# Kernel tuning notes

Measured on AMD Instinct MI355X. Metric: run time of the kernel, lower is better.

Reference implementation:

```python
import jax, jax.numpy as jnp
import numpy as np

B, T, D, H = 64, 1024, 512, 512

def setup_inputs() -> dict:
    key = jax.random.key(0)
    k1, k2, k3, k4 = jax.random.split(key, 4)
    x = jax.random.normal(k1, (B, T, D), dtype=jnp.float32)
    # Keras LSTM weights: kernel [D, 4H], recurrent_kernel [H, 4H], bias [4H]
    # gate order: i, f, c(g), o
    kernel = jax.random.normal(k2, (D, 4 * H), dtype=jnp.float32) * 0.05
    recurrent_kernel = jax.random.normal(k3, (H, 4 * H), dtype=jnp.float32) * 0.05
    bias = jax.random.normal(k4, (4 * H,), dtype=jnp.float32) * 0.05
    return {"x": x, "kernel": kernel, "recurrent_kernel": recurrent_kernel, "bias": bias}

def reference(x, kernel, recurrent_kernel, bias):
    # Precompute input projections for all timesteps: [B, T, 4H]
    xW = jnp.einsum('btd,dg->btg', x, kernel) + bias
    xW_t = jnp.transpose(xW, (1, 0, 2))  # [T, B, 4H] for scan over time
    h0 = jnp.zeros((x.shape[0], recurrent_kernel.shape[0]), dtype=x.dtype)
    c0 = jnp.zeros_like(h0)

    def step(carry, xw):
        h, c = carry
        z = xw + h @ recurrent_kernel  # [B, 4H]
        i, f, g, o = jnp.split(z, 4, axis=-1)
        i = jax.nn.sigmoid(i)
        f = jax.nn.sigmoid(f)
        g = jnp.tanh(g)
        o = jax.nn.sigmoid(o)
        c_new = f * c + i * g
        h_new = o * jnp.tanh(c_new)
        return (h_new, c_new), None

    (h_final, _), _ = jax.lax.scan(step, (h0, c0), xW_t)
    return h_final  # [B, H]
```

## Files before the change

### kernel.cpp

```cpp
#include <hip/hip_runtime.h>


#define B_  64
#define T_  1024
#define D_  512
#define H_  512
#define G4H 2048

typedef _Float16 half8 __attribute__((ext_vector_type(8)));
typedef _Float16 half4 __attribute__((ext_vector_type(4)));
typedef float    f32x4 __attribute__((ext_vector_type(4)));
typedef unsigned long long ull;
typedef unsigned int u32;

static __device__ __forceinline__ float sigm(float x) { return 1.f / (1.f + __expf(-x)); }
static __device__ __forceinline__ float tanh_(float x) {
    float xc = fminf(fmaxf(x, -15.f), 15.f);
    float e  = __expf(2.f * xc);
    return (e - 1.f) / (e + 1.f);
}
static __device__ __forceinline__ float lo16f(unsigned u) {
    return (float)__builtin_bit_cast(_Float16, (unsigned short)(u & 0xffffu));
}
static __device__ __forceinline__ float hi16f(unsigned u) {
    return (float)__builtin_bit_cast(_Float16, (unsigned short)(u >> 16));
}
static __device__ __forceinline__ void gload_lds16(const _Float16* g, _Float16* l) {
    __builtin_amdgcn_global_load_lds((const __attribute__((address_space(1))) u32*)g,
                                     (__attribute__((address_space(3))) u32*)l, 16, 0, 0);
}

__global__ void trans_w(const float* __restrict__ W, _Float16* __restrict__ WT) {
    int idx = blockIdx.x * blockDim.x + threadIdx.x;
    int total = D_ * G4H;
    int stride = gridDim.x * blockDim.x;
    for (int i = idx; i < total; i += stride) {
        int k = i >> 11;
        int n = i & (G4H - 1);
        WT[(size_t)n * D_ + k] = (_Float16)W[i];
    }
}

__global__ void conv_x(const float* __restrict__ x, _Float16* __restrict__ xh) {
    int idx = blockIdx.x * blockDim.x + threadIdx.x;
    int total = (B_ * T_ * D_) / 4;
    int stride = gridDim.x * blockDim.x;
    const f32x4* xi = (const f32x4*)x;
    half4* xo = (half4*)xh;
    for (int i = idx; i < total; i += stride) {
        f32x4 v = xi[i];
        xo[i] = (half4){(_Float16)v.x, (_Float16)v.y, (_Float16)v.z, (_Float16)v.w};
    }
}

__global__ void zero_buf(unsigned* __restrict__ p, int n) {
    int idx = blockIdx.x * blockDim.x + threadIdx.x;
    int stride = gridDim.x * blockDim.x;
    for (int i = idx; i < n; i += stride) p[i] = 0u;
}

__global__ __launch_bounds__(256) void gemm_xw_f16(const _Float16* __restrict__ xh,
                                                   const _Float16* __restrict__ WkT,
                                                   const float* __restrict__ bias,
                                                   _Float16* __restrict__ xw, int tbase) {
    __shared__ _Float16 As[128 * 64];
    __shared__ _Float16 Bs[128 * 64];
    const int tid  = threadIdx.x;
    const int lane = tid & 63;
    const int wave = tid >> 6;
    const int l15  = lane & 15;
    const int quad = lane >> 4;
    const int b     = blockIdx.z;
    const int n0    = blockIdx.x * 128;
    const int tloc0 = blockIdx.y * 128;

    const int srow = tid >> 3;
    const int sseg = tid & 7;

    f32x4 acc[2][8];
#pragma unroll
    for (int rt = 0; rt < 2; ++rt)
#pragma unroll
        for (int ct = 0; ct < 8; ++ct) acc[rt][ct] = (f32x4){0.f, 0.f, 0.f, 0.f};

    const _Float16* abase = xh + ((size_t)b * T_ + tbase + tloc0) * D_;
    const _Float16* bbase = WkT + (size_t)n0 * D_;

    for (int kb = 0; kb < 8; ++kb) {
        __syncthreads();
#pragma unroll
        for (int q = 0; q < 4; ++q) {
            int row  = q * 32 + srow;
            int col2 = (sseg * 16) ^ ((row & 7) << 4);
            _Float16* ldst = (_Float16*)((char*)As + q * 4096 + wave * 1024);
            gload_lds16(abase + (size_t)row * D_ + kb * 64 + (col2 >> 1), ldst);
            _Float16* ldstb = (_Float16*)((char*)Bs + q * 4096 + wave * 1024);
            gload_lds16(bbase + (size_t)row * D_ + kb * 64 + (col2 >> 1), ldstb);
        }
        __syncthreads();
#pragma unroll
        for (int ks = 0; ks < 2; ++ks) {
            half8 af[2];
#pragma unroll
            for (int rt = 0; rt < 2; ++rt) {
                int row = wave * 32 + rt * 16 + l15;
                int c2  = (ks * 64 + quad * 16) ^ ((row & 7) << 4);
                af[rt] = *(const half8*)&As[row * 64 + (c2 >> 1)];
            }
#pragma unroll
            for (int ct = 0; ct < 8; ++ct) {
                int brw = ct * 16 + l15;
                int c2  = (ks * 64 + quad * 16) ^ ((brw & 7) << 4);
                half8 bf = *(const half8*)&Bs[brw * 64 + (c2 >> 1)];
                acc[0][ct] = __builtin_amdgcn_mfma_f32_16x16x32_f16(af[0], bf, acc[0][ct], 0, 0, 0);
                acc[1][ct] = __builtin_amdgcn_mfma_f32_16x16x32_f16(af[1], bf, acc[1][ct], 0, 0, 0);
            }
        }
    }
#pragma unroll
    for (int ct = 0; ct < 8; ++ct) {
        int col = n0 + ct * 16 + l15;
        float bs = bias[col];
#pragma unroll
        for (int rt = 0; rt < 2; ++rt)
#pragma unroll
            for (int r = 0; r < 4; ++r) {
                int tt = tloc0 + wave * 32 + rt * 16 + quad * 4 + r;
                xw[((size_t)tt * B_ + b) * G4H + col] = (_Float16)(acc[rt][ct][r] + bs);
            }
    }
}

__global__ __launch_bounds__(256) void gemm_xw_small(const float* __restrict__ x,
                                                     const _Float16* __restrict__ WkT,
                                                     const float* __restrict__ bias,
                                                     _Float16* __restrict__ xw,
                                                     int tbase) {
    __shared__ _Float16 As[64][40];
    __shared__ _Float16 Bst[64][40];
    const int tid  = threadIdx.x;
    const int lane = tid & 63;
    const int wave = tid >> 6;
    const int l15  = lane & 15;
    const int quad = lane >> 4;
    const int b     = blockIdx.z;
    const int n0    = blockIdx.x * 64;
    const int tloc0 = blockIdx.y * 64;

    const float* xbase = x + ((size_t)b * T_ + (tbase + tloc0)) * D_;
    f32x4 acc[4];
#pragma unroll
    for (int i = 0; i < 4; ++i) acc[i] = (f32x4){0.f, 0.f, 0.f, 0.f};

    const int ai = tid >> 2, ac = tid & 3;
    const int bn = tid >> 2, bq = tid & 3;

    for (int kb = 0; kb < 16; ++kb) {
        __syncthreads();
        const float* ap = xbase + (size_t)ai * D_ + kb * 32 + ac * 8;
        f32x4 av0 = *(const f32x4*)ap;
        f32x4 av1 = *(const f32x4*)(ap + 4);
        half8 ah = { (_Float16)av0.x, (_Float16)av0.y, (_Float16)av0.z, (_Float16)av0.w,
                     (_Float16)av1.x, (_Float16)av1.y, (_Float16)av1.z, (_Float16)av1.w };
        *(half8*)&As[ai][ac * 8] = ah;
        half8 bv = *(const half8*)(WkT + (size_t)(n0 + bn) * D_ + kb * 32 + bq * 8);
        *(half8*)&Bst[bn][bq * 8] = bv;
        __syncthreads();

        half8 afrag = *(const half8*)&As[16 * wave + l15][quad * 8];
#pragma unroll
        for (int nt = 0; nt < 4; ++nt) {
            half8 bfrag = *(const half8*)&Bst[nt * 16 + l15][quad * 8];
            acc[nt] = __builtin_amdgcn_mfma_f32_16x16x32_f16(afrag, bfrag, acc[nt], 0, 0, 0);
        }
    }
#pragma unroll
    for (int nt = 0; nt < 4; ++nt)
#pragma unroll
        for (int r = 0; r < 4; ++r) {
            int tt  = tloc0 + 16 * wave + quad * 4 + r;
            int col = n0 + nt * 16 + l15;
            xw[((size_t)tt * B_ + b) * G4H + col] = (_Float16)(acc[nt][r] + bias[col]);
        }
}

__global__ __launch_bounds__(256, 1) void lstm_scan(const _Float16* __restrict__ xw,
                                                    const _Float16* __restrict__ WrT,
                                                    unsigned* __restrict__ hbuf,
                                                    float* __restrict__ cio,
                                                    float* __restrict__ out,
                                                    int t0, int t1) {
    const int w    = blockIdx.x;
    const int g    = w & 3;
    const int s    = w >> 2;
    const int u0   = s * 32;
    const int tid  = threadIdx.x;
    const int lane = tid & 63;
    const int wave = tid >> 6;
    const int l15  = lane & 15;
    const int quad = lane >> 4;

    half8 bfrag[2][16];
#pragma unroll
    for (int ct = 0; ct < 2; ++ct) {
        const int col = wave * H_ + u0 + ct * 16 + l15;
        const _Float16* wp = WrT + (size_t)col * D_;
#pragma unroll
        for (int kt = 0; kt < 16; ++kt)
            bfrag[ct][kt] = *(const half8*)(wp + kt * 32 + quad * 8);
    }

    const int rho  = tid >> 4;
    const int jj   = tid & 15;
    const int brow = g * 16 + rho;
    const int un0  = u0 + 2 * jj;
    float c0 = 0.f, c1 = 0.f;
    if (t0 != 0) {
        c0 = cio[(size_t)brow * H_ + un0];
        c1 = cio[(size_t)brow * H_ + un0 + 1];
    }

    __shared__ _Float16 hS[16][520];
    __shared__ float    zS[16][4][34];

    const size_t slotSz = (size_t)B_ * H_;

    for (int t = t0; t < t1; ++t) {
        const unsigned* xwd = (const unsigned*)(xw + ((size_t)(t - t0) * B_ + brow) * G4H);
        const int dbase = (u0 >> 1) + jj;
        unsigned xwi = xwd[0 * 256 + dbase];
        unsigned xwf = xwd[1 * 256 + dbase];
        unsigned xwg = xwd[2 * 256 + dbase];
        unsigned xwo = xwd[3 * 256 + dbase];

        if (t > 0) {
            const ull* src = (const ull*)(hbuf + (size_t)((t - 1) % 3) * slotSz)
                             + (size_t)(g * 16) * 256 + tid;
            const unsigned tgt = (unsigned)(t & 0xffff);
            const ull expect = ((ull)tgt << 16) | ((ull)tgt << 48);
            ull v[16];
            int guard = 0;
            while (true) {
                ull diff = 0;
#pragma unroll
                for (int k = 0; k < 16; ++k)
                    v[k] = __hip_atomic_load(src + (size_t)k * 256,
                                             __ATOMIC_RELAXED, __HIP_MEMORY_SCOPE_AGENT);
#pragma unroll
                for (int k = 0; k < 16; ++k)
                    diff |= (v[k] ^ expect) & 0xffff0000ffff0000ull;
                if (diff == 0) break;
                if (++guard > 8192) break;
            }
#pragma unroll
            for (int k = 0; k < 16; ++k) {
                unsigned p = (unsigned)(v[k] & 0xffffu) | (((unsigned)(v[k] >> 32)) << 16);
                *(unsigned*)&hS[k][2 * tid] = p;
            }
        }
        __syncthreads();

        f32x4 a0 = {0.f,0.f,0.f,0.f}, a1 = a0, b0 = a0, b1 = a0;
        if (t > 0) {
#pragma unroll
            for (int kt = 0; kt < 16; kt += 2) {
                half8 af0 = *(const half8*)&hS[l15][kt * 32 + quad * 8];
                half8 af1 = *(const half8*)&hS[l15][(kt + 1) * 32 + quad * 8];
                a0 = __builtin_amdgcn_mfma_f32_16x16x32_f16(af0, bfrag[0][kt],     a0, 0, 0, 0);
                a1 = __builtin_amdgcn_mfma_f32_16x16x32_f16(af0, bfrag[1][kt],     a1, 0, 0, 0);
                b0 = __builtin_amdgcn_mfma_f32_16x16x32_f16(af1, bfrag[0][kt + 1], b0, 0, 0, 0);
                b1 = __builtin_amdgcn_mfma_f32_16x16x32_f16(af1, bfrag[1][kt + 1], b1, 0, 0, 0);
            }
        }
        f32x4 z0 = a0 + b0, z1 = a1 + b1;
#pragma unroll
        for (int r = 0; r < 4; ++r) {
            zS[quad * 4 + r][wave][l15]      = z0[r];
            zS[quad * 4 + r][wave][16 + l15] = z1[r];
        }
        __syncthreads();

        float zi0 = zS[rho][0][2*jj] + lo16f(xwi), zi1 = zS[rho][0][2*jj+1] + hi16f(xwi);
        float zf0 = zS[rho][1][2*jj] + lo16f(xwf), zf1 = zS[rho][1][2*jj+1] + hi16f(xwf);
        float zg0 = zS[rho][2][2*jj] + lo16f(xwg), zg1 = zS[rho][2][2*jj+1] + hi16f(xwg);
        float zo0 = zS[rho][3][2*jj] + lo16f(xwo), zo1 = zS[rho][3][2*jj+1] + hi16f(xwo);

        c0 = sigm(zf0) * c0 + sigm(zi0) * tanh_(zg0);
        c1 = sigm(zf1) * c1 + sigm(zi1) * tanh_(zg1);
        float h0 = sigm(zo0) * tanh_(c0);
        float h1 = sigm(zo1) * tanh_(c1);

        const unsigned tagw = ((unsigned)((t + 1) & 0xffff)) << 16;
        unsigned d0 = (unsigned)__builtin_bit_cast(unsigned short, (_Float16)h0) | tagw;
        unsigned d1 = (unsigned)__builtin_bit_cast(unsigned short, (_Float16)h1) | tagw;
        ull wv = (ull)d0 | ((ull)d1 << 32);
        __hip_atomic_store((ull*)(hbuf + (size_t)(t % 3) * slotSz) + (size_t)brow * 256 + (un0 >> 1),
                           wv, __ATOMIC_RELAXED, __HIP_MEMORY_SCOPE_AGENT);

        if (t == T_ - 1) {
            out[(size_t)brow * H_ + un0]     = h0;
            out[(size_t)brow * H_ + un0 + 1] = h1;
        }
    }
    cio[(size_t)brow * H_ + un0]     = c0;
    cio[(size_t)brow * H_ + un0 + 1] = c1;
}

extern "C" void kernel_launch(void* const* d_in, const int* in_sizes, int n_in,
                              void* d_out, int out_size, void* d_ws, size_t ws_size,
                              hipStream_t stream) {
    (void)in_sizes; (void)n_in;
    const float* x    = (const float*)d_in[0];
    const float* Wk   = (const float*)d_in[1];
    const float* Wr   = (const float*)d_in[2];
    const float* bias = (const float*)d_in[3];
    float* out = (float*)d_out;

    char* ws = (char*)d_ws;
    _Float16* WkT  = (_Float16*)(ws + 1024);
    _Float16* WrT  = (_Float16*)(ws + 1024 + 2097152);
    unsigned* hbuf = (unsigned*)(ws + 1024 + 2 * 2097152);
    float*    cio  = (float*)(ws + 1024 + 2 * 2097152 + 393216);
    const size_t fixed   = 1024 + 2 * 2097152 + 393216 + 131072;
    const size_t xhBytes = (size_t)B_ * T_ * D_ * 2;
    const size_t perT    = (size_t)B_ * G4H * 2;

    size_t avail = (ws_size > fixed) ? ws_size - fixed : 0;
    bool use_xh = avail >= xhBytes + 128 * perT;
    _Float16* xh = (_Float16*)(ws + fixed);
    _Float16* xw = (_Float16*)(ws + fixed + (use_xh ? xhBytes : 0));

    int ct = 0;
    if (use_xh) {
        const int cands[4] = {1024, 512, 256, 128};
        size_t av2 = avail - xhBytes;
        for (int i = 0; i < 4; ++i)
            if ((size_t)cands[i] * perT <= av2) { ct = cands[i]; break; }
    } else {
        const int cands[5] = {1024, 512, 256, 128, 64};
        for (int i = 0; i < 5; ++i)
            if ((size_t)cands[i] * perT <= avail) { ct = cands[i]; break; }
    }
    if (ct == 0) {
        hipMemsetAsync(d_out, 0, (size_t)out_size * 4, stream);
        return;
    }

    zero_buf<<<96, 256, 0, stream>>>(hbuf, 3 * B_ * H_);
    trans_w<<<512, 256, 0, stream>>>(Wk, WkT);
    trans_w<<<512, 256, 0, stream>>>(Wr, WrT);
    if (use_xh) conv_x<<<2048, 256, 0, stream>>>(x, xh);

    for (int t0 = 0; t0 < T_; t0 += ct) {
        if (use_xh)
            gemm_xw_f16<<<dim3(16, ct / 128, B_), 256, 0, stream>>>(xh, WkT, bias, xw, t0);
        else
            gemm_xw_small<<<dim3(32, ct / 64, B_), 256, 0, stream>>>(x, WkT, bias, xw, t0);
        lstm_scan<<<64, 256, 0, stream>>>(xw, WrT, hbuf, cio, out, t0, t0 + ct);
    }
}
```

Baseline: 3.167 ms.

## Split LSTM scan across 128 blocks with 8 batch rows each and inline-asm polling

Doubles the number of scan workgroups from 64 to 128. Each block now owns 8 batch rows instead of 16, so every thread handles one hidden unit and polls only 8 hidden-state words per step. The MFMA tiles are padded with zeroed LDS rows, so half of the matrix math is wasted on padding. Polling uses inline-asm sc0 loads and falls back to atomic loads if it spins too long. The per-step wait per block shrinks, but the recurrent-weight fragments are now loaded by twice as many blocks and cross-block synchronisation traffic goes up.

```diff
diff --git a/kernel.cpp b/kernel.cpp
--- a/kernel.cpp
+++ b/kernel.cpp
@@ -18,12 +18,6 @@
     float xc = fminf(fmaxf(x, -15.f), 15.f);
     float e  = __expf(2.f * xc);
     return (e - 1.f) / (e + 1.f);
-}
-static __device__ __forceinline__ float lo16f(unsigned u) {
-    return (float)__builtin_bit_cast(_Float16, (unsigned short)(u & 0xffffu));
-}
-static __device__ __forceinline__ float hi16f(unsigned u) {
-    return (float)__builtin_bit_cast(_Float16, (unsigned short)(u >> 16));
 }
 static __device__ __forceinline__ void gload_lds16(const _Float16* g, _Float16* l) {
     __builtin_amdgcn_global_load_lds((const __attribute__((address_space(1))) u32*)g,
@@ -191,8 +185,8 @@
                                                     float* __restrict__ out,
                                                     int t0, int t1) {
     const int w    = blockIdx.x;
-    const int g    = w & 3;
-    const int s    = w >> 2;
+    const int g    = w & 7;
+    const int s    = w >> 3;
     const int u0   = s * 32;
     const int tid  = threadIdx.x;
     const int lane = tid & 63;
@@ -210,53 +204,84 @@
             bfrag[ct][kt] = *(const half8*)(wp + kt * 32 + quad * 8);
     }
 
-    const int rho  = tid >> 4;
-    const int jj   = tid & 15;
-    const int brow = g * 16 + rho;
-    const int un0  = u0 + 2 * jj;
-    float c0 = 0.f, c1 = 0.f;
-    if (t0 != 0) {
-        c0 = cio[(size_t)brow * H_ + un0];
-        c1 = cio[(size_t)brow * H_ + un0 + 1];
-    }
+    const int rho  = tid >> 5;
+    const int uu   = tid & 31;
+    const int brow = g * 8 + rho;
+    const int un   = u0 + uu;
+    float c = 0.f;
+    if (t0 != 0) c = cio[(size_t)brow * H_ + un];
 
     __shared__ _Float16 hS[16][520];
-    __shared__ float    zS[16][4][34];
+    __shared__ float    zS[8][4][34];
+
+    for (int i = tid; i < 8 * 520; i += 256) ((_Float16*)&hS[8][0])[i] = (_Float16)0.f;
+    __syncthreads();
 
     const size_t slotSz = (size_t)B_ * H_;
+    bool fastok = true;
 
     for (int t = t0; t < t1; ++t) {
-        const unsigned* xwd = (const unsigned*)(xw + ((size_t)(t - t0) * B_ + brow) * G4H);
-        const int dbase = (u0 >> 1) + jj;
-        unsigned xwi = xwd[0 * 256 + dbase];
-        unsigned xwf = xwd[1 * 256 + dbase];
-        unsigned xwg = xwd[2 * 256 + dbase];
-        unsigned xwo = xwd[3 * 256 + dbase];
+        const _Float16* xwp = xw + ((size_t)(t - t0) * B_ + brow) * G4H + un;
+        float xi_ = (float)xwp[0 * 512];
+        float xf_ = (float)xwp[1 * 512];
+        float xg_ = (float)xwp[2 * 512];
+        float xo_ = (float)xwp[3 * 512];
 
         if (t > 0) {
             const ull* src = (const ull*)(hbuf + (size_t)((t - 1) % 3) * slotSz)
-                             + (size_t)(g * 16) * 256 + tid;
+                             + (size_t)(g * 8) * 256 + tid;
             const unsigned tgt = (unsigned)(t & 0xffff);
             const ull expect = ((ull)tgt << 16) | ((ull)tgt << 48);
-            ull v[16];
-            int guard = 0;
-            while (true) {
-                ull diff = 0;
-#pragma unroll
-                for (int k = 0; k < 16; ++k)
-                    v[k] = __hip_atomic_load(src + (size_t)k * 256,
-                                             __ATOMIC_RELAXED, __HIP_MEMORY_SCOPE_AGENT);
-#pragma unroll
-                for (int k = 0; k < 16; ++k)
-                    diff |= (v[k] ^ expect) & 0xffff0000ffff0000ull;
-                if (diff == 0) break;
-                if (++guard > 8192) break;
-            }
-#pragma unroll
-            for (int k = 0; k < 16; ++k) {
-                unsigned p = (unsigned)(v[k] & 0xffffu) | (((unsigned)(v[k] >> 32)) << 16);
-                *(unsigned*)&hS[k][2 * tid] = p;
-            }
+            ull v0 = 0, v1 = 0, v2 = 0, v3 = 0, v4 = 0, v5 = 0, v6 = 0, v7 = 0;
+            bool got = false;
+            if (fastok) {
+                int guard = 0;
+                while (true) {
+                    asm volatile(
+                        "global_load_dwordx2 %0, %8, off sc0\n\t"
+                        "global_load_dwordx2 %1, %9, off sc0\n\t"
+                        "global_load_dwordx2 %2, %10, off sc0\n\t"
+                        "global_load_dwordx2 %3, %11, off sc0\n\t"
+                        "global_load_dwordx2 %4, %12, off sc0\n\t"
+                        "global_load_dwordx2 %5, %13, off sc0\n\t"
+                        "global_load_dwordx2 %6, %14, off sc0\n\t"
+                        "global_load_dwordx2 %7, %15, off sc0\n\t"
+                        "s_waitcnt vmcnt(0)"
+                        : "=&v"(v0), "=&v"(v1), "=&v"(v2), "=&v"(v3),
+                          "=&v"(v4), "=&v"(v5), "=&v"(v6), "=&v"(v7)
+                        : "v"(src), "v"(src + 256), "v"(src + 512), "v"(src + 768),
+                          "v"(src + 1024), "v"(src + 1280), "v"(src + 1536), "v"(src + 1792)
+                        : "memory");
+                    ull diff = ((v0 ^ expect) | (v1 ^ expect) | (v2 ^ expect) | (v3 ^ expect)
+                              | (v4 ^ expect) | (v5 ^ expect) | (v6 ^ expect) | (v7 ^ expect))
+                              & 0xffff0000ffff0000ull;
+                    if (diff == 0) { got = true; break; }
+                    if (++guard > 512) { fastok = false; break; }
+                }
+            }
+            if (!got) {
+                int guard = 0;
+                while (true) {
+                    v0 = __hip_atomic_load(src + 0,    __ATOMIC_RELAXED, __HIP_MEMORY_SCOPE_AGENT);
+                    v1 = __hip_atomic_load(src + 256,  __ATOMIC_RELAXED, __HIP_MEMORY_SCOPE_AGENT);
+                    v2 = __hip_atomic_load(src + 512,  __ATOMIC_RELAXED, __HIP_MEMORY_SCOPE_AGENT);
+                    v3 = __hip_atomic_load(src + 768,  __ATOMIC_RELAXED, __HIP_MEMORY_SCOPE_AGENT);
+                    v4 = __hip_atomic_load(src + 1024, __ATOMIC_RELAXED, __HIP_MEMORY_SCOPE_AGENT);
+                    v5 = __hip_atomic_load(src + 1280, __ATOMIC_RELAXED, __HIP_MEMORY_SCOPE_AGENT);
+                    v6 = __hip_atomic_load(src + 1536, __ATOMIC_RELAXED, __HIP_MEMORY_SCOPE_AGENT);
+                    v7 = __hip_atomic_load(src + 1792, __ATOMIC_RELAXED, __HIP_MEMORY_SCOPE_AGENT);
+                    ull diff = ((v0 ^ expect) | (v1 ^ expect) | (v2 ^ expect) | (v3 ^ expect)
+                              | (v4 ^ expect) | (v5 ^ expect) | (v6 ^ expect) | (v7 ^ expect))
+                              & 0xffff0000ffff0000ull;
+                    if (diff == 0) break;
+                    if (++guard > 4096) break;
+                }
+            }
+#define STG(k_, vk_) *(unsigned*)&hS[k_][2 * tid] = \
+        (unsigned)((vk_) & 0xffffu) | ((unsigned)((vk_) >> 32) << 16);
+            STG(0, v0) STG(1, v1) STG(2, v2) STG(3, v3)
+            STG(4, v4) STG(5, v5) STG(6, v6) STG(7, v7)
+#undef STG
         }
         __syncthreads();
 
@@ -273,37 +298,32 @@
             }
         }
         f32x4 z0 = a0 + b0, z1 = a1 + b1;
-#pragma unroll
-        for (int r = 0; r < 4; ++r) {
-            zS[quad * 4 + r][wave][l15]      = z0[r];
-            zS[quad * 4 + r][wave][16 + l15] = z1[r];
-        }
-        __syncthreads();
-
-        float zi0 = zS[rho][0][2*jj] + lo16f(xwi), zi1 = zS[rho][0][2*jj+1] + hi16f(xwi);
-        float zf0 = zS[rho][1][2*jj] + lo16f(xwf), zf1 = zS[rho][1][2*jj+1] + hi16f(xwf);
-        float zg0 = zS[rho][2][2*jj] + lo16f(xwg), zg1 = zS[rho][2][2*jj+1] + hi16f(xwg);
-        float zo0 = zS[rho][3][2*jj] + lo16f(xwo), zo1 = zS[rho][3][2*jj+1] + hi16f(xwo);
-
-        c0 = sigm(zf0) * c0 + sigm(zi0) * tanh_(zg0);
-        c1 = sigm(zf1) * c1 + sigm(zi1) * tanh_(zg1);
-        float h0 = sigm(zo0) * tanh_(c0);
-        float h1 = sigm(zo1) * tanh_(c1);
-
-        const unsigned tagw = ((unsigned)((t + 1) & 0xffff)) << 16;
-        unsigned d0 = (unsigned)__builtin_bit_cast(unsigned short, (_Float16)h0) | tagw;
-        unsigned d1 = (unsigned)__builtin_bit_cast(unsigned short, (_Float16)h1) | tagw;
-        ull wv = (ull)d0 | ((ull)d1 << 32);
-        __hip_atomic_store((ull*)(hbuf + (size_t)(t % 3) * slotSz) + (size_t)brow * 256 + (un0 >> 1),
-                           wv, __ATOMIC_RELAXED, __HIP_MEMORY_SCOPE_AGENT);
-
-        if (t == T_ - 1) {
-            out[(size_t)brow * H_ + un0]     = h0;
-            out[(size_t)brow * H_ + un0 + 1] = h1;
-        }
-    }
-    cio[(size_t)brow * H_ + un0]     = c0;
-    cio[(size_t)brow * H_ + un0 + 1] = c1;
+        if (quad < 2) {
+#pragma unroll
+            for (int r = 0; r < 4; ++r) {
+                zS[quad * 4 + r][wave][l15]      = z0[r];
+                zS[quad * 4 + r][wave][16 + l15] = z1[r];
+            }
+        }
+        __syncthreads();
+
+        float zi = zS[rho][0][uu] + xi_;
+        float zf = zS[rho][1][uu] + xf_;
+        float zg = zS[rho][2][uu] + xg_;
+        float zo = zS[rho][3][uu] + xo_;
+
+        c = sigm(zf) * c + sigm(zi) * tanh_(zg);
+        float h = sigm(zo) * tanh_(c);
+
+        unsigned d = (unsigned)__builtin_bit_cast(unsigned short, (_Float16)h)
+                   | (((unsigned)((t + 1) & 0xffff)) << 16);
+        unsigned* dst = hbuf + (size_t)(t % 3) * slotSz + (size_t)brow * H_ + un;
+        __hip_atomic_store(dst, d, __ATOMIC_RELAXED, __HIP_MEMORY_SCOPE_AGENT);
+        asm volatile("global_store_dword %0, %1, off sc0" :: "v"(dst), "v"(d) : "memory");
+
+        if (t == T_ - 1) out[(size_t)brow * H_ + un] = h;
+    }
+    cio[(size_t)brow * H_ + un] = c;
 }
 
 extern "C" void kernel_launch(void* const* d_in, const int* in_sizes, int n_in,
@@ -356,6 +376,6 @@
             gemm_xw_f16<<<dim3(16, ct / 128, B_), 256, 0, stream>>>(xh, WkT, bias, xw, t0);
         else
             gemm_xw_small<<<dim3(32, ct / 64, B_), 256, 0, stream>>>(x, WkT, bias, xw, t0);
-        lstm_scan<<<64, 256, 0, stream>>>(xw, WrT, hbuf, cio, out, t0, t0 + ct);
-    }
-}
+        lstm_scan<<<128, 256, 0, stream>>>(xw, WrT, hbuf, cio, out, t0, t0 + ct);
+    }
+}
```

Result: slower. 4.588 ms (+44.9%).

## Repartition LSTM scan into 16 workgroups of 1024 threads sharing own h locally

Applied to the files above, without the earlier changes.

The recurrent scan moves from 64 workgroups of 256 threads to 16 workgroups of 1024 threads. Each workgroup now owns 128 hidden units for 16 batch rows, so a quarter of the next h vector is written straight into LDS. Only the other three quarters are polled from global memory through the tagged atomic buffer. This is meant to cut cross-workgroup global polling traffic and sync latency per timestep, at the cost of fewer CUs and more threads per barrier.

```diff
diff --git a/kernel.cpp b/kernel.cpp
--- a/kernel.cpp
+++ b/kernel.cpp
@@ -184,36 +184,37 @@
         }
 }
 
-__global__ __launch_bounds__(256, 1) void lstm_scan(const _Float16* __restrict__ xw,
-                                                    const _Float16* __restrict__ WrT,
-                                                    unsigned* __restrict__ hbuf,
-                                                    float* __restrict__ cio,
-                                                    float* __restrict__ out,
-                                                    int t0, int t1) {
+__global__ __launch_bounds__(1024, 1) void lstm_scan(const _Float16* __restrict__ xw,
+                                                     const _Float16* __restrict__ WrT,
+                                                     unsigned* __restrict__ hbuf,
+                                                     float* __restrict__ cio,
+                                                     float* __restrict__ out,
+                                                     int t0, int t1) {
     const int w    = blockIdx.x;
-    const int g    = w & 3;
-    const int s    = w >> 2;
-    const int u0   = s * 32;
+    const int g    = w >> 2;
+    const int q    = w & 3;
     const int tid  = threadIdx.x;
     const int lane = tid & 63;
     const int wave = tid >> 6;
     const int l15  = lane & 15;
     const int quad = lane >> 4;
+    const int u    = wave >> 1;
+    const int hf   = wave & 1;
 
     half8 bfrag[2][16];
 #pragma unroll
     for (int ct = 0; ct < 2; ++ct) {
-        const int col = wave * H_ + u0 + ct * 16 + l15;
+        const int col = (2 * hf + ct) * H_ + q * 128 + u * 16 + l15;
         const _Float16* wp = WrT + (size_t)col * D_;
 #pragma unroll
         for (int kt = 0; kt < 16; ++kt)
             bfrag[ct][kt] = *(const half8*)(wp + kt * 32 + quad * 8);
     }
 
-    const int rho  = tid >> 4;
-    const int jj   = tid & 15;
+    const int rho  = wave;
+    const int jj   = lane;
     const int brow = g * 16 + rho;
-    const int un0  = u0 + 2 * jj;
+    const int un0  = q * 128 + 2 * jj;
     float c0 = 0.f, c1 = 0.f;
     if (t0 != 0) {
         c0 = cio[(size_t)brow * H_ + un0];
@@ -221,41 +222,55 @@
     }
 
     __shared__ _Float16 hS[16][520];
-    __shared__ float    zS[16][4][34];
+    __shared__ float    zS[16][4][136];
 
     const size_t slotSz = (size_t)B_ * H_;
+
+    int upm[3];
+#pragma unroll
+    for (int m = 0; m < 3; ++m) {
+        int idx = jj + 64 * m;
+        upm[m] = idx + ((idx >= q * 64) ? 64 : 0);
+    }
 
     for (int t = t0; t < t1; ++t) {
         const unsigned* xwd = (const unsigned*)(xw + ((size_t)(t - t0) * B_ + brow) * G4H);
-        const int dbase = (u0 >> 1) + jj;
+        const int dbase = q * 64 + jj;
         unsigned xwi = xwd[0 * 256 + dbase];
         unsigned xwf = xwd[1 * 256 + dbase];
         unsigned xwg = xwd[2 * 256 + dbase];
         unsigned xwo = xwd[3 * 256 + dbase];
 
         if (t > 0) {
-            const ull* src = (const ull*)(hbuf + (size_t)((t - 1) % 3) * slotSz)
-                             + (size_t)(g * 16) * 256 + tid;
+            const ull* srcb = (const ull*)(hbuf + (size_t)((t - 1) % 3) * slotSz)
+                              + (size_t)brow * 256;
             const unsigned tgt = (unsigned)(t & 0xffff);
             const ull expect = ((ull)tgt << 16) | ((ull)tgt << 48);
-            ull v[16];
+            ull v0 = 0, v1 = 0, v2 = 0;
             int guard = 0;
             while (true) {
-                ull diff = 0;
-#pragma unroll
-                for (int k = 0; k < 16; ++k)
-                    v[k] = __hip_atomic_load(src + (size_t)k * 256,
-                                             __ATOMIC_RELAXED, __HIP_MEMORY_SCOPE_AGENT);
-#pragma unroll
-                for (int k = 0; k < 16; ++k)
-                    diff |= (v[k] ^ expect) & 0xffff0000ffff0000ull;
+                v0 = __hip_atomic_load(srcb + upm[0], __ATOMIC_RELAXED, __HIP_MEMORY_SCOPE_AGENT);
+                v1 = __hip_atomic_load(srcb + upm[1], __ATOMIC_RELAXED, __HIP_MEMORY_SCOPE_AGENT);
+                v2 = __hip_atomic_load(srcb + upm[2], __ATOMIC_RELAXED, __HIP_MEMORY_SCOPE_AGENT);
+                ull diff = ((v0 ^ expect) | (v1 ^ expect) | (v2 ^ expect))
+                           & 0xffff0000ffff0000ull;
                 if (diff == 0) break;
                 if (++guard > 8192) break;
             }
-#pragma unroll
-            for (int k = 0; k < 16; ++k) {
-                unsigned p = (unsigned)(v[k] & 0xffffu) | (((unsigned)(v[k] >> 32)) << 16);
-                *(unsigned*)&hS[k][2 * tid] = p;
+            if (t == t0) {
+                ull vo; int gd = 0;
+                do {
+                    vo = __hip_atomic_load(srcb + (q * 64 + jj),
+                                           __ATOMIC_RELAXED, __HIP_MEMORY_SCOPE_AGENT);
+                } while (((vo ^ expect) & 0xffff0000ffff0000ull) && ++gd < 8192);
+                *(unsigned*)&hS[rho][2 * (q * 64 + jj)] =
+                    (unsigned)(vo & 0xffffu) | ((unsigned)(vo >> 32) << 16);
+            }
+#pragma unroll
+            for (int m = 0; m < 3; ++m) {
+                ull vk = (m == 0) ? v0 : (m == 1) ? v1 : v2;
+                *(unsigned*)&hS[rho][2 * upm[m]] =
+                    (unsigned)(vk & 0xffffu) | ((unsigned)(vk >> 32) << 16);
             }
         }
         __syncthreads();
@@ -275,8 +290,8 @@
         f32x4 z0 = a0 + b0, z1 = a1 + b1;
 #pragma unroll
         for (int r = 0; r < 4; ++r) {
-            zS[quad * 4 + r][wave][l15]      = z0[r];
-            zS[quad * 4 + r][wave][16 + l15] = z1[r];
+            zS[quad * 4 + r][2 * hf][u * 16 + l15]     = z0[r];
+            zS[quad * 4 + r][2 * hf + 1][u * 16 + l15] = z1[r];
         }
         __syncthreads();
 
@@ -290,11 +305,14 @@
         float h0 = sigm(zo0) * tanh_(c0);
         float h1 = sigm(zo1) * tanh_(c1);
 
+        unsigned h0b = (unsigned)__builtin_bit_cast(unsigned short, (_Float16)h0);
+        unsigned h1b = (unsigned)__builtin_bit_cast(unsigned short, (_Float16)h1);
+        *(unsigned*)&hS[rho][2 * (q * 64 + jj)] = h0b | (h1b << 16);
+
         const unsigned tagw = ((unsigned)((t + 1) & 0xffff)) << 16;
-        unsigned d0 = (unsigned)__builtin_bit_cast(unsigned short, (_Float16)h0) | tagw;
-        unsigned d1 = (unsigned)__builtin_bit_cast(unsigned short, (_Float16)h1) | tagw;
-        ull wv = (ull)d0 | ((ull)d1 << 32);
-        __hip_atomic_store((ull*)(hbuf + (size_t)(t % 3) * slotSz) + (size_t)brow * 256 + (un0 >> 1),
+        ull wv = (ull)(h0b | tagw) | (((ull)(h1b | tagw)) << 32);
+        __hip_atomic_store((ull*)(hbuf + (size_t)(t % 3) * slotSz)
+                               + (size_t)brow * 256 + (q * 64 + jj),
                            wv, __ATOMIC_RELAXED, __HIP_MEMORY_SCOPE_AGENT);
 
         if (t == T_ - 1) {
@@ -356,6 +374,6 @@
             gemm_xw_f16<<<dim3(16, ct / 128, B_), 256, 0, stream>>>(xh, WkT, bias, xw, t0);
         else
             gemm_xw_small<<<dim3(32, ct / 64, B_), 256, 0, stream>>>(x, WkT, bias, xw, t0);
-        lstm_scan<<<64, 256, 0, stream>>>(xw, WrT, hbuf, cio, out, t0, t0 + ct);
-    }
-}
+        lstm_scan<<<16, 1024, 0, stream>>>(xw, WrT, hbuf, cio, out, t0, t0 + ct);
+    }
+}
```

Measured after the change: 9.354 ms. 195% more time.

## Double scan block threads to 512 so each wave handles one MFMA column tile

Applied to the files above, without the earlier changes.

The recurrent scan kernel now runs 8 waves per block instead of 4. Each wave owns one gate/column-tile pair, so its serial MFMA chain per step drops from 32 to 16 instructions. Each thread also handles one hidden unit instead of two, and the polling loads per thread are halved. This shortens per-step latency in the latency-bound recurrence, at the cost of more threads contending at the barriers and more spin-polling traffic on the shared h buffer.

```diff
diff --git a/kernel.cpp b/kernel.cpp
--- a/kernel.cpp
+++ b/kernel.cpp
@@ -18,12 +18,6 @@
     float xc = fminf(fmaxf(x, -15.f), 15.f);
     float e  = __expf(2.f * xc);
     return (e - 1.f) / (e + 1.f);
-}
-static __device__ __forceinline__ float lo16f(unsigned u) {
-    return (float)__builtin_bit_cast(_Float16, (unsigned short)(u & 0xffffu));
-}
-static __device__ __forceinline__ float hi16f(unsigned u) {
-    return (float)__builtin_bit_cast(_Float16, (unsigned short)(u >> 16));
 }
 static __device__ __forceinline__ void gload_lds16(const _Float16* g, _Float16* l) {
     __builtin_amdgcn_global_load_lds((const __attribute__((address_space(1))) u32*)g,
@@ -184,7 +178,7 @@
         }
 }
 
-__global__ __launch_bounds__(256, 1) void lstm_scan(const _Float16* __restrict__ xw,
+__global__ __launch_bounds__(512, 1) void lstm_scan(const _Float16* __restrict__ xw,
                                                     const _Float16* __restrict__ WrT,
                                                     unsigned* __restrict__ hbuf,
                                                     float* __restrict__ cio,
@@ -199,111 +193,95 @@
     const int wave = tid >> 6;
     const int l15  = lane & 15;
     const int quad = lane >> 4;
-
-    half8 bfrag[2][16];
-#pragma unroll
-    for (int ct = 0; ct < 2; ++ct) {
-        const int col = wave * H_ + u0 + ct * 16 + l15;
+    const int gt   = wave >> 1;
+    const int ctw  = wave & 1;
+
+    half8 bfrag[16];
+    {
+        const int col = gt * H_ + u0 + ctw * 16 + l15;
         const _Float16* wp = WrT + (size_t)col * D_;
 #pragma unroll
         for (int kt = 0; kt < 16; ++kt)
-            bfrag[ct][kt] = *(const half8*)(wp + kt * 32 + quad * 8);
-    }
-
-    const int rho  = tid >> 4;
-    const int jj   = tid & 15;
+            bfrag[kt] = *(const half8*)(wp + kt * 32 + quad * 8);
+    }
+
+    const int rho  = tid >> 5;
+    const int uu   = tid & 31;
     const int brow = g * 16 + rho;
-    const int un0  = u0 + 2 * jj;
-    float c0 = 0.f, c1 = 0.f;
-    if (t0 != 0) {
-        c0 = cio[(size_t)brow * H_ + un0];
-        c1 = cio[(size_t)brow * H_ + un0 + 1];
-    }
+    const int un   = u0 + uu;
+    float c = 0.f;
+    if (t0 != 0) c = cio[(size_t)brow * H_ + un];
 
     __shared__ _Float16 hS[16][520];
-    __shared__ float    zS[16][4][34];
+    __shared__ float    zS[16][4][35];
 
     const size_t slotSz = (size_t)B_ * H_;
+    const int pp = tid & 255;
+    const int rh = tid >> 8;
 
     for (int t = t0; t < t1; ++t) {
-        const unsigned* xwd = (const unsigned*)(xw + ((size_t)(t - t0) * B_ + brow) * G4H);
-        const int dbase = (u0 >> 1) + jj;
-        unsigned xwi = xwd[0 * 256 + dbase];
-        unsigned xwf = xwd[1 * 256 + dbase];
-        unsigned xwg = xwd[2 * 256 + dbase];
-        unsigned xwo = xwd[3 * 256 + dbase];
+        const _Float16* xwp = xw + ((size_t)(t - t0) * B_ + brow) * G4H + un;
+        float xi_ = (float)xwp[0 * 512];
+        float xf_ = (float)xwp[1 * 512];
+        float xg_ = (float)xwp[2 * 512];
+        float xo_ = (float)xwp[3 * 512];
 
         if (t > 0) {
             const ull* src = (const ull*)(hbuf + (size_t)((t - 1) % 3) * slotSz)
-                             + (size_t)(g * 16) * 256 + tid;
+                             + (size_t)(g * 16 + rh * 8) * 256 + pp;
             const unsigned tgt = (unsigned)(t & 0xffff);
             const ull expect = ((ull)tgt << 16) | ((ull)tgt << 48);
-            ull v[16];
+            ull v[8];
             int guard = 0;
             while (true) {
                 ull diff = 0;
 #pragma unroll
-                for (int k = 0; k < 16; ++k)
+                for (int k = 0; k < 8; ++k)
                     v[k] = __hip_atomic_load(src + (size_t)k * 256,
                                              __ATOMIC_RELAXED, __HIP_MEMORY_SCOPE_AGENT);
 #pragma unroll
-                for (int k = 0; k < 16; ++k)
+                for (int k = 0; k < 8; ++k)
                     diff |= (v[k] ^ expect) & 0xffff0000ffff0000ull;
                 if (diff == 0) break;
                 if (++guard > 8192) break;
             }
 #pragma unroll
-            for (int k = 0; k < 16; ++k) {
+            for (int k = 0; k < 8; ++k) {
                 unsigned p = (unsigned)(v[k] & 0xffffu) | (((unsigned)(v[k] >> 32)) << 16);
-                *(unsigned*)&hS[k][2 * tid] = p;
-            }
-        }
-        __syncthreads();
-
-        f32x4 a0 = {0.f,0.f,0.f,0.f}, a1 = a0, b0 = a0, b1 = a0;
+                *(unsigned*)&hS[rh * 8 + k][2 * pp] = p;
+            }
+        }
+        __syncthreads();
+
+        f32x4 a = {0.f, 0.f, 0.f, 0.f};
         if (t > 0) {
 #pragma unroll
-            for (int kt = 0; kt < 16; kt += 2) {
-                half8 af0 = *(const half8*)&hS[l15][kt * 32 + quad * 8];
-                half8 af1 = *(const half8*)&hS[l15][(kt + 1) * 32 + quad * 8];
-                a0 = __builtin_amdgcn_mfma_f32_16x16x32_f16(af0, bfrag[0][kt],     a0, 0, 0, 0);
-                a1 = __builtin_amdgcn_mfma_f32_16x16x32_f16(af0, bfrag[1][kt],     a1, 0, 0, 0);
-                b0 = __builtin_amdgcn_mfma_f32_16x16x32_f16(af1, bfrag[0][kt + 1], b0, 0, 0, 0);
-                b1 = __builtin_amdgcn_mfma_f32_16x16x32_f16(af1, bfrag[1][kt + 1], b1, 0, 0, 0);
-            }
-        }
-        f32x4 z0 = a0 + b0, z1 = a1 + b1;
-#pragma unroll
-        for (int r = 0; r < 4; ++r) {
-            zS[quad * 4 + r][wave][l15]      = z0[r];
-            zS[quad * 4 + r][wave][16 + l15] = z1[r];
-        }
-        __syncthreads();
-
-        float zi0 = zS[rho][0][2*jj] + lo16f(xwi), zi1 = zS[rho][0][2*jj+1] + hi16f(xwi);
-        float zf0 = zS[rho][1][2*jj] + lo16f(xwf), zf1 = zS[rho][1][2*jj+1] + hi16f(xwf);
-        float zg0 = zS[rho][2][2*jj] + lo16f(xwg), zg1 = zS[rho][2][2*jj+1] + hi16f(xwg);
-        float zo0 = zS[rho][3][2*jj] + lo16f(xwo), zo1 = zS[rho][3][2*jj+1] + hi16f(xwo);
-
-        c0 = sigm(zf0) * c0 + sigm(zi0) * tanh_(zg0);
-        c1 = sigm(zf1) * c1 + sigm(zi1) * tanh_(zg1);
-        float h0 = sigm(zo0) * tanh_(c0);
-        float h1 = sigm(zo1) * tanh_(c1);
-
-        const unsigned tagw = ((unsigned)((t + 1) & 0xffff)) << 16;
-        unsigned d0 = (unsigned)__builtin_bit_cast(unsigned short, (_Float16)h0) | tagw;
-        unsigned d1 = (unsigned)__builtin_bit_cast(unsigned short, (_Float16)h1) | tagw;
-        ull wv = (ull)d0 | ((ull)d1 << 32);
-        __hip_atomic_store((ull*)(hbuf + (size_t)(t % 3) * slotSz) + (size_t)brow * 256 + (un0 >> 1),
-                           wv, __ATOMIC_RELAXED, __HIP_MEMORY_SCOPE_AGENT);
-
-        if (t == T_ - 1) {
-            out[(size_t)brow * H_ + un0]     = h0;
-            out[(size_t)brow * H_ + un0 + 1] = h1;
-        }
-    }
-    cio[(size_t)brow * H_ + un0]     = c0;
-    cio[(size_t)brow * H_ + un0 + 1] = c1;
+            for (int kt = 0; kt < 16; ++kt) {
+                half8 af = *(const half8*)&hS[l15][kt * 32 + quad * 8];
+                a = __builtin_amdgcn_mfma_f32_16x16x32_f16(af, bfrag[kt], a, 0, 0, 0);
+            }
+        }
+#pragma unroll
+        for (int r = 0; r < 4; ++r)
+            zS[quad * 4 + r][gt][ctw * 16 + l15] = a[r];
+        __syncthreads();
+
+        float zi = zS[rho][0][uu] + xi_;
+        float zf = zS[rho][1][uu] + xf_;
+        float zg = zS[rho][2][uu] + xg_;
+        float zo = zS[rho][3][uu] + xo_;
+
+        c = sigm(zf) * c + sigm(zi) * tanh_(zg);
+        float h = sigm(zo) * tanh_(c);
+
+        unsigned d = (unsigned)__builtin_bit_cast(unsigned short, (_Float16)h)
+                   | (((unsigned)((t + 1) & 0xffff)) << 16);
+        __hip_atomic_store(hbuf + (size_t)(t % 3) * slotSz + (size_t)brow * H_ + un,
+                           d, __ATOMIC_RELAXED, __HIP_MEMORY_SCOPE_AGENT);
+
+        if (t == T_ - 1) out[(size_t)brow * H_ + un] = h;
+    }
+    cio[(size_t)brow * H_ + un] = c;
 }
 
 extern "C" void kernel_launch(void* const* d_in, const int* in_sizes, int n_in,
@@ -356,6 +334,6 @@
             gemm_xw_f16<<<dim3(16, ct / 128, B_), 256, 0, stream>>>(xh, WkT, bias, xw, t0);
         else
             gemm_xw_small<<<dim3(32, ct / 64, B_), 256, 0, stream>>>(x, WkT, bias, xw, t0);
-        lstm_scan<<<64, 256, 0, stream>>>(xw, WrT, hbuf, cio, out, t0, t0 + ct);
-    }
-}
+        lstm_scan<<<64, 512, 0, stream>>>(xw, WrT, hbuf, cio, out, t0, t0 + ct);
+    }
+}
```

After: 3.384 ms. 6.9% more time.
